# Kernel tuning notes

Hardware: AMD Instinct MI355X
Metric: run time of the kernel (lower is better)

Reference implementation:

```python
import jax, jax.numpy as jnp
import numpy as np

IN_NC, OUT_NC, K = 64, 64, 3          # adc_in_nc, adc_out_nc, adc_kers
FC_SIZE = 512
FMN0, FMN1 = 512, 512
GROUP_FC = 4
CNN_PARA = IN_NC * OUT_NC * K * K + OUT_NC  # 36928
B, H, W = 16, 128, 128


def setup_inputs() -> dict:
    key = jax.random.key(0)
    ks = jax.random.split(key, 8)
    s = 0.05
    return {
        "x": jax.random.normal(ks[0], (B, IN_NC, H, W), jnp.float32),
        "fc_in": jax.random.normal(ks[1], (B, FC_SIZE), jnp.float32),
        "w1": jax.random.normal(ks[2], (FMN0, FC_SIZE), jnp.float32) * s,
        "b1": jax.random.normal(ks[3], (FMN0,), jnp.float32) * s,
        "w2": jax.random.normal(ks[4], (FMN1, FMN0), jnp.float32) * s,
        "b2": jax.random.normal(ks[5], (FMN1,), jnp.float32) * s,
        # grouped 1x1 conv1d: [groups, out_per_group, in_per_group]
        "w3": jax.random.normal(ks[6], (GROUP_FC, CNN_PARA // GROUP_FC, FMN1 // GROUP_FC), jnp.float32) * s,
        "b3": jax.random.normal(ks[7], (CNN_PARA,), jnp.float32) * s,
        "splits": B,
    }


def _fmn(fc_in, w1, b1, w2, b2, w3, b3):
    # per-sample MLP (Conv1d with kernel 1 over length-1 sequence)
    h = jax.nn.relu(fc_in @ w1.T + b1)                      # [B, FMN0]
    h = jax.nn.relu(h @ w2.T + b2)                          # [B, FMN1]
    hg = h.reshape(h.shape[0], GROUP_FC, -1)                # [B, G, FMN1/G]
    o = jnp.einsum('bgi,goi->bgo', hg, w3)                  # [B, G, CNN_PARA/G]
    o = o.reshape(h.shape[0], -1) + b3                      # [B, CNN_PARA]
    return jax.nn.relu(o)


def reference(x, fc_in, w1, b1, w2, b2, w3, b3, splits):
    batch, C, Hx, Wx = x.shape
    wb = _fmn(fc_in, w1, b1, w2, b2, w3, b3)                # [B, CNN_PARA]
    weight = wb[:, :-OUT_NC].reshape(splits * OUT_NC, IN_NC, K, K)
    bias = wb[:, -OUT_NC:].reshape(-1)                      # [B*OUT_NC]
    # per-sample conv via grouped conv (groups = batch), VALID padding, stride 1
    y = jax.lax.conv_general_dilated(
        x.reshape(1, batch * C, Hx, Wx), weight,
        window_strides=(1, 1), padding='VALID',
        feature_group_count=batch,
        dimension_numbers=('NCHW', 'OIHW', 'NCHW'))          # [1, B*OUT, H', W']
    y = y + bias[None, :, None, None]
    # match torch conv3d output shape [1, B*OUT, 1, H', W']
    return y.reshape(1, batch * OUT_NC, 1, y.shape[-2], y.shape[-1])
```

## Files before the change

### kernel.cpp

```cpp
#include <hip/hip_runtime.h>
#include <hip/hip_bf16.h>

constexpr int BATCH   = 16;
constexpr int IN_NC   = 64;
constexpr int OUT_NC  = 64;
constexpr int KS      = 3;
constexpr int FC      = 512;
constexpr int GROUPS  = 4;
constexpr int CNN_PARA = IN_NC * OUT_NC * KS * KS + OUT_NC;
constexpr int PER_G   = CNN_PARA / GROUPS;
constexpr int IN_PER_G = FC / GROUPS;
constexpr int H = 128, W = 128;
constexpr int HO = 126, WO = 126;
constexpr int PIX = HO * WO;
constexpr int WCOUNT = IN_NC * OUT_NC * KS * KS;
constexpr int HW = H * W;

typedef __attribute__((ext_vector_type(8))) short short8;
typedef __attribute__((ext_vector_type(4))) float f32x4;

static __device__ __forceinline__ short bf16_bits(float f) {
    __hip_bfloat16 h = __float2bfloat16(f);
    union { __hip_bfloat16 h; short s; } u; u.h = h;
    return u.s;
}

__global__ __launch_bounds__(256) void mlp_layer(
    const float* __restrict__ in, const float* __restrict__ w,
    const float* __restrict__ bias, float* __restrict__ out)
{
    int gtid = blockIdx.x * blockDim.x + threadIdx.x;
    int wave = gtid >> 6;
    int lane = threadIdx.x & 63;
    if (wave >= BATCH * FC) return;
    int b = wave >> 9;
    int o = wave & (FC - 1);
    const float* in_row = in + b * FC;
    const float* w_row  = w + (size_t)o * FC;
    float acc = 0.f;
#pragma unroll
    for (int i = 0; i < FC / 64; ++i) acc += in_row[lane + i * 64] * w_row[lane + i * 64];
#pragma unroll
    for (int off = 32; off > 0; off >>= 1) acc += __shfl_down(acc, off, 64);
    if (lane == 0) {
        float v = acc + bias[o];
        out[b * FC + o] = v > 0.f ? v : 0.f;
    }
}

__global__ __launch_bounds__(256) void grouped_fc(
    const float* __restrict__ h2, const float* __restrict__ w3,
    const float* __restrict__ b3, float* __restrict__ wb)
{
    __shared__ float hs[BATCH * FC];
    int tid = threadIdx.x;
    for (int i = tid; i < BATCH * FC; i += blockDim.x) hs[i] = h2[i];
    __syncthreads();

    int j = blockIdx.x * blockDim.x + tid;
    if (j >= CNN_PARA) return;
    int g  = j / PER_G;
    int jj = j - g * PER_G;
    const float4* wrow = (const float4*)(w3 + ((size_t)g * PER_G + jj) * IN_PER_G);
    float acc[BATCH];
#pragma unroll
    for (int b = 0; b < BATCH; ++b) acc[b] = 0.f;
    const float* hbase = hs + g * IN_PER_G;
#pragma unroll 4
    for (int i4 = 0; i4 < IN_PER_G / 4; ++i4) {
        float4 wv = wrow[i4];
#pragma unroll
        for (int b = 0; b < BATCH; ++b) {
            const float* hb = hbase + b * FC + i4 * 4;
            acc[b] += wv.x * hb[0] + wv.y * hb[1] + wv.z * hb[2] + wv.w * hb[3];
        }
    }
    float bv = b3[j];
#pragma unroll
    for (int b = 0; b < BATCH; ++b) {
        float v = acc[b] + bv;
        wb[(size_t)b * CNN_PARA + j] = v > 0.f ? v : 0.f;
    }
}

__global__ __launch_bounds__(256) void conv_w_transpose(
    const float* __restrict__ wb, __hip_bfloat16* __restrict__ wT)
{
    int idx = blockIdx.x * blockDim.x + threadIdx.x;
    if (idx >= BATCH * 9 * 64 * 64) return;
    int b    = idx / (9 * 4096);
    int r    = idx % (9 * 4096);
    int kykx = r >> 12;
    int q    = r & 4095;
    int oc   = q >> 6;
    int ic   = q & 63;
    float v = wb[(size_t)b * CNN_PARA + (oc * 64 + ic) * 9 + kykx];
    union { __hip_bfloat16 h; short s; } u; u.s = bf16_bits(v);
    wT[idx] = u.h;
}

__global__ __launch_bounds__(256) void conv_x_transpose(
    const float* __restrict__ x, __hip_bfloat16* __restrict__ xT)
{
    __shared__ float lds[64][129];
    int blk = blockIdx.x;
    int b = blk >> 7, h = blk & 127;
    int tid = threadIdx.x;

    const float* xrow = x + (size_t)b * IN_NC * HW + (size_t)h * W;
#pragma unroll 8
    for (int it = 0; it < 32; ++it) {
        int ic = it * 2 + (tid >> 7);
        int w  = tid & 127;
        lds[ic][w] = xrow[(size_t)ic * HW + w];
    }
    __syncthreads();

    __hip_bfloat16* dst = xT + ((size_t)(b * 128 + h)) * (128 * 64);
#pragma unroll
    for (int i = 0; i < 4; ++i) {
        int chunk = i * 256 + tid;
        int w = chunk >> 3, oct = chunk & 7;
        short8 v;
#pragma unroll
        for (int j = 0; j < 8; ++j) v[j] = bf16_bits(lds[oct * 8 + j][w]);
        *(short8*)(dst + (size_t)w * 64 + oct * 8) = v;
    }
}

__global__ __launch_bounds__(256) void conv_mfma(
    const __hip_bfloat16* __restrict__ xT,
    const __hip_bfloat16* __restrict__ wT,
    const float* __restrict__ wb,
    float* __restrict__ out)
{
    int blk = blockIdx.x;
    int b   = blk / 63;
    int oyp = blk % 63;
    int tid = threadIdx.x;
    int wv = tid >> 6, l = tid & 63;
    int mrow  = wv & 1;
    int nhalf = wv >> 1;
    int row = oyp * 2 + nhalf;
    int l15 = l & 15, l4 = l >> 4;

    f32x4 acc[2][8];
#pragma unroll
    for (int mf = 0; mf < 2; ++mf)
#pragma unroll
        for (int nf = 0; nf < 8; ++nf) acc[mf][nf] = (f32x4)0.f;

#pragma unroll
    for (int kykx = 0; kykx < 9; ++kykx) {
        int ky = kykx / 3, kx = kykx % 3;
        const __hip_bfloat16* wtile = wT + (size_t)(b * 9 + kykx) * 4096;
        const __hip_bfloat16* xbase =
            xT + ((size_t)(b * 128 + row + ky) * 128 + kx) * 64;
#pragma unroll
        for (int ks = 0; ks < 2; ++ks) {
            int ic0 = ks * 32 + l4 * 8;
            short8 a0 = *(const short8*)(wtile + (mrow * 32 + l15) * 64 + ic0);
            short8 a1 = *(const short8*)(wtile + (mrow * 32 + 16 + l15) * 64 + ic0);
#pragma unroll
            for (int nf = 0; nf < 8; ++nf) {
                int ox = nf * 16 + l15;
                short8 bf = *(const short8*)(xbase + (size_t)ox * 64 + ic0);
                acc[0][nf] = __builtin_amdgcn_mfma_f32_16x16x32_bf16(a0, bf, acc[0][nf], 0, 0, 0);
                acc[1][nf] = __builtin_amdgcn_mfma_f32_16x16x32_bf16(a1, bf, acc[1][nf], 0, 0, 0);
            }
        }
    }

    float bias[2][4];
#pragma unroll
    for (int mf = 0; mf < 2; ++mf)
#pragma unroll
        for (int r = 0; r < 4; ++r)
            bias[mf][r] = wb[(size_t)b * CNN_PARA + WCOUNT + mrow * 32 + mf * 16 + l4 * 4 + r];

#pragma unroll
    for (int mf = 0; mf < 2; ++mf)
#pragma unroll
        for (int nf = 0; nf < 8; ++nf) {
            int ox = nf * 16 + l15;
            if (ox >= WO) continue;
#pragma unroll
            for (int r = 0; r < 4; ++r) {
                int oc = mrow * 32 + mf * 16 + l4 * 4 + r;
                out[((size_t)(b * 64 + oc)) * PIX + row * WO + ox] = acc[mf][nf][r] + bias[mf][r];
            }
        }
}

__global__ __launch_bounds__(256) void conv_direct(
    const float* __restrict__ x, const float* __restrict__ wb,
    float* __restrict__ out)
{
    constexpr int NBLK = (PIX + 255) / 256;
    __shared__ float wsm[IN_NC * 9];
    __shared__ float bias_s;
    int bid  = blockIdx.x;
    int tile = bid % NBLK;
    int boc  = bid / NBLK;
    int b = boc >> 6, oc = boc & 63;
    int tid = threadIdx.x;
    const float* wsrc = wb + (size_t)b * CNN_PARA + oc * (IN_NC * 9);
    if (tid < IN_NC * 9 / 4) ((float4*)wsm)[tid] = ((const float4*)wsrc)[tid];
    if (tid == 0) bias_s = wb[(size_t)b * CNN_PARA + WCOUNT + oc];
    __syncthreads();
    int p = tile * 256 + tid;
    if (p >= PIX) return;
    int oy = p / WO, ox = p - oy * WO;
    const float* xb = x + (size_t)b * IN_NC * HW + oy * W + ox;
    float acc = bias_s;
    for (int ic = 0; ic < IN_NC; ++ic) {
        const float* xr = xb + ic * HW;
        const float* wr = wsm + ic * 9;
#pragma unroll
        for (int ky = 0; ky < 3; ++ky) {
            acc += xr[ky * W + 0] * wr[ky * 3 + 0];
            acc += xr[ky * W + 1] * wr[ky * 3 + 1];
            acc += xr[ky * W + 2] * wr[ky * 3 + 2];
        }
    }
    out[(size_t)boc * PIX + p] = acc;
}

extern "C" void kernel_launch(void* const* d_in, const int* in_sizes, int n_in,
                              void* d_out, int out_size, void* d_ws, size_t ws_size,
                              hipStream_t stream) {
    const float* x     = (const float*)d_in[0];
    const float* fc_in = (const float*)d_in[1];
    const float* w1    = (const float*)d_in[2];
    const float* b1    = (const float*)d_in[3];
    const float* w2    = (const float*)d_in[4];
    const float* b2    = (const float*)d_in[5];
    const float* w3    = (const float*)d_in[6];
    const float* b3    = (const float*)d_in[7];
    float* out = (float*)d_out;

    const size_t off_h1 = 0;
    const size_t off_h2 = off_h1 + (size_t)BATCH * FC * 4;
    const size_t off_wb = off_h2 + (size_t)BATCH * FC * 4;
    const size_t off_wT = off_wb + (size_t)BATCH * CNN_PARA * 4;
    const size_t off_xT = off_wT + (size_t)BATCH * 9 * 4096 * 2;
    const size_t xT_bytes = (size_t)BATCH * 128 * 128 * 64 * 2 + 16384;
    const size_t need = off_xT + xT_bytes;

    float* h1 = (float*)((char*)d_ws + off_h1);
    float* h2 = (float*)((char*)d_ws + off_h2);
    float* wb = (float*)((char*)d_ws + off_wb);

    mlp_layer<<<2048, 256, 0, stream>>>(fc_in, w1, b1, h1);
    mlp_layer<<<2048, 256, 0, stream>>>(h1, w2, b2, h2);
    grouped_fc<<<(CNN_PARA + 255) / 256, 256, 0, stream>>>(h2, w3, b3, wb);

    if (ws_size >= need) {
        __hip_bfloat16* wT = (__hip_bfloat16*)((char*)d_ws + off_wT);
        __hip_bfloat16* xT = (__hip_bfloat16*)((char*)d_ws + off_xT);
        conv_w_transpose<<<(BATCH * 9 * 4096 + 255) / 256, 256, 0, stream>>>(wb, wT);
        conv_x_transpose<<<BATCH * 128, 256, 0, stream>>>(x, xT);
        conv_mfma<<<BATCH * 63, 256, 0, stream>>>(xT, wT, wb, out);
    } else {
        conv_direct<<<BATCH * OUT_NC * ((PIX + 255) / 256), 256, 0, stream>>>(x, wb, out);
    }
}
```

Baseline: 270.6 us.

## Restructure MLP kernels for batch reuse and retile conv MFMA with XCD swizzle

The MLP layers now stage all batch activations in shared memory and have each wave compute one output neuron for all 16 samples, so each weight row is read once instead of once per sample. The grouped FC switches to a wave-per-output layout with coalesced weight loads and shuffle reductions. The conv MFMA kernel changes from a 2x8 to a 4x4 fragment tile per wave to improve operand reuse, adds an occupancy hint, and remaps block indices across XCDs. This brings more shuffle reductions, launches one block per four outputs in grouped_fc, and adds register pressure in the conv kernel.

```diff
diff --git a/kernel.cpp b/kernel.cpp
--- a/kernel.cpp
+++ b/kernel.cpp
@@ -20,66 +20,83 @@
 typedef __attribute__((ext_vector_type(4))) float f32x4;
 
 static __device__ __forceinline__ short bf16_bits(float f) {
-    __hip_bfloat16 h = __float2bfloat16(f);
-    union { __hip_bfloat16 h; short s; } u; u.h = h;
+    union { __hip_bfloat16 h; short s; } u;
+    u.h = __float2bfloat16(f);
     return u.s;
 }
 
 __global__ __launch_bounds__(256) void mlp_layer(
-    const float* __restrict__ in, const float* __restrict__ w,
-    const float* __restrict__ bias, float* __restrict__ out)
-{
-    int gtid = blockIdx.x * blockDim.x + threadIdx.x;
-    int wave = gtid >> 6;
-    int lane = threadIdx.x & 63;
-    if (wave >= BATCH * FC) return;
-    int b = wave >> 9;
-    int o = wave & (FC - 1);
-    const float* in_row = in + b * FC;
-    const float* w_row  = w + (size_t)o * FC;
-    float acc = 0.f;
-#pragma unroll
-    for (int i = 0; i < FC / 64; ++i) acc += in_row[lane + i * 64] * w_row[lane + i * 64];
-#pragma unroll
-    for (int off = 32; off > 0; off >>= 1) acc += __shfl_down(acc, off, 64);
-    if (lane == 0) {
-        float v = acc + bias[o];
-        out[b * FC + o] = v > 0.f ? v : 0.f;
+    const float* __restrict__ in,
+    const float* __restrict__ w,
+    const float* __restrict__ bias,
+    float* __restrict__ out)
+{
+    __shared__ float hs[BATCH * FC];
+    int tid = threadIdx.x;
+    for (int i = tid; i < BATCH * FC; i += 256) hs[i] = in[i];
+    __syncthreads();
+
+    int o = blockIdx.x * 4 + (tid >> 6);
+    int l = tid & 63;
+    const float4* wrow = (const float4*)(w + (size_t)o * FC + l * 8);
+    float4 w0 = wrow[0], w1 = wrow[1];
+
+    float acc[BATCH];
+#pragma unroll
+    for (int b = 0; b < BATCH; ++b) {
+        const float4* hp = (const float4*)(hs + b * FC + l * 8);
+        float4 h0 = hp[0], h1 = hp[1];
+        acc[b] = w0.x * h0.x + w0.y * h0.y + w0.z * h0.z + w0.w * h0.w
+               + w1.x * h1.x + w1.y * h1.y + w1.z * h1.z + w1.w * h1.w;
+    }
+#pragma unroll
+    for (int off = 32; off > 0; off >>= 1)
+#pragma unroll
+        for (int b = 0; b < BATCH; ++b)
+            acc[b] += __shfl_down(acc[b], off, 64);
+    if (l == 0) {
+        float bv = bias[o];
+#pragma unroll
+        for (int b = 0; b < BATCH; ++b) {
+            float v = acc[b] + bv;
+            out[b * FC + o] = v > 0.f ? v : 0.f;
+        }
     }
 }
 
 __global__ __launch_bounds__(256) void grouped_fc(
-    const float* __restrict__ h2, const float* __restrict__ w3,
-    const float* __restrict__ b3, float* __restrict__ wb)
+    const float* __restrict__ h2,
+    const float* __restrict__ w3,
+    const float* __restrict__ b3,
+    float* __restrict__ wb)
 {
     __shared__ float hs[BATCH * FC];
     int tid = threadIdx.x;
-    for (int i = tid; i < BATCH * FC; i += blockDim.x) hs[i] = h2[i];
-    __syncthreads();
-
-    int j = blockIdx.x * blockDim.x + tid;
-    if (j >= CNN_PARA) return;
-    int g  = j / PER_G;
-    int jj = j - g * PER_G;
-    const float4* wrow = (const float4*)(w3 + ((size_t)g * PER_G + jj) * IN_PER_G);
+    for (int i = tid; i < BATCH * FC; i += 256) hs[i] = h2[i];
+    __syncthreads();
+
+    int j = blockIdx.x * 4 + (tid >> 6);
+    int l = tid & 63;
+    int g = j / PER_G;
+    const float2 wv = *(const float2*)(w3 + (size_t)j * IN_PER_G + l * 2);
+    const float* hbase = hs + g * IN_PER_G + l * 2;
+
     float acc[BATCH];
 #pragma unroll
-    for (int b = 0; b < BATCH; ++b) acc[b] = 0.f;
-    const float* hbase = hs + g * IN_PER_G;
-#pragma unroll 4
-    for (int i4 = 0; i4 < IN_PER_G / 4; ++i4) {
-        float4 wv = wrow[i4];
+    for (int b = 0; b < BATCH; ++b)
+        acc[b] = wv.x * hbase[b * FC] + wv.y * hbase[b * FC + 1];
+#pragma unroll
+    for (int off = 32; off > 0; off >>= 1)
+#pragma unroll
+        for (int b = 0; b < BATCH; ++b)
+            acc[b] += __shfl_down(acc[b], off, 64);
+    if (l == 0) {
+        float bv = b3[j];
 #pragma unroll
         for (int b = 0; b < BATCH; ++b) {
-            const float* hb = hbase + b * FC + i4 * 4;
-            acc[b] += wv.x * hb[0] + wv.y * hb[1] + wv.z * hb[2] + wv.w * hb[3];
-        }
-    }
-    float bv = b3[j];
-#pragma unroll
-    for (int b = 0; b < BATCH; ++b) {
-        float v = acc[b] + bv;
-        wb[(size_t)b * CNN_PARA + j] = v > 0.f ? v : 0.f;
+            float v = acc[b] + bv;
+            wb[(size_t)b * CNN_PARA + j] = v > 0.f ? v : 0.f;
+        }
     }
 }
 
@@ -87,7 +104,7 @@
     const float* __restrict__ wb, __hip_bfloat16* __restrict__ wT)
 {
     int idx = blockIdx.x * blockDim.x + threadIdx.x;
-    if (idx >= BATCH * 9 * 64 * 64) return;
+    if (idx >= BATCH * 9 * 4096) return;
     int b    = idx / (9 * 4096);
     int r    = idx % (9 * 4096);
     int kykx = r >> 12;
@@ -128,66 +145,72 @@
     }
 }
 
-__global__ __launch_bounds__(256) void conv_mfma(
+__global__ __launch_bounds__(256, 4) void conv_mfma(
     const __hip_bfloat16* __restrict__ xT,
     const __hip_bfloat16* __restrict__ wT,
     const float* __restrict__ wb,
     float* __restrict__ out)
 {
-    int blk = blockIdx.x;
-    int b   = blk / 63;
-    int oyp = blk % 63;
+    int wg   = blockIdx.x;
+    int sblk = (wg & 7) * 126 + (wg >> 3);
+    int b    = sblk / 63;
+    int rp   = sblk % 63;
+
     int tid = threadIdx.x;
     int wv = tid >> 6, l = tid & 63;
-    int mrow  = wv & 1;
-    int nhalf = wv >> 1;
-    int row = oyp * 2 + nhalf;
     int l15 = l & 15, l4 = l >> 4;
-
-    f32x4 acc[2][8];
-#pragma unroll
-    for (int mf = 0; mf < 2; ++mf)
-#pragma unroll
-        for (int nf = 0; nf < 8; ++nf) acc[mf][nf] = (f32x4)0.f;
+    int row = rp * 2 + (wv >> 1);
+    int px0 = (wv & 1) * 64;
+
+    f32x4 acc[4][4];
+#pragma unroll
+    for (int mf = 0; mf < 4; ++mf)
+#pragma unroll
+        for (int nf = 0; nf < 4; ++nf) acc[mf][nf] = (f32x4)0.f;
 
 #pragma unroll
     for (int kykx = 0; kykx < 9; ++kykx) {
         int ky = kykx / 3, kx = kykx % 3;
         const __hip_bfloat16* wtile = wT + (size_t)(b * 9 + kykx) * 4096;
-        const __hip_bfloat16* xbase =
+        const __hip_bfloat16* xrow =
             xT + ((size_t)(b * 128 + row + ky) * 128 + kx) * 64;
 #pragma unroll
         for (int ks = 0; ks < 2; ++ks) {
             int ic0 = ks * 32 + l4 * 8;
-            short8 a0 = *(const short8*)(wtile + (mrow * 32 + l15) * 64 + ic0);
-            short8 a1 = *(const short8*)(wtile + (mrow * 32 + 16 + l15) * 64 + ic0);
-#pragma unroll
-            for (int nf = 0; nf < 8; ++nf) {
-                int ox = nf * 16 + l15;
-                short8 bf = *(const short8*)(xbase + (size_t)ox * 64 + ic0);
-                acc[0][nf] = __builtin_amdgcn_mfma_f32_16x16x32_bf16(a0, bf, acc[0][nf], 0, 0, 0);
-                acc[1][nf] = __builtin_amdgcn_mfma_f32_16x16x32_bf16(a1, bf, acc[1][nf], 0, 0, 0);
+            short8 A[4];
+#pragma unroll
+            for (int mf = 0; mf < 4; ++mf)
+                A[mf] = *(const short8*)(wtile + (mf * 16 + l15) * 64 + ic0);
+#pragma unroll
+            for (int nf = 0; nf < 4; ++nf) {
+                int ox = px0 + nf * 16 + l15;
+                short8 bf = *(const short8*)(xrow + (size_t)ox * 64 + ic0);
+#pragma unroll
+                for (int mf = 0; mf < 4; ++mf)
+                    acc[mf][nf] = __builtin_amdgcn_mfma_f32_16x16x32_bf16(
+                        A[mf], bf, acc[mf][nf], 0, 0, 0);
             }
         }
     }
 
-    float bias[2][4];
-#pragma unroll
-    for (int mf = 0; mf < 2; ++mf)
+    float bias[4][4];
+#pragma unroll
+    for (int mf = 0; mf < 4; ++mf)
 #pragma unroll
         for (int r = 0; r < 4; ++r)
-            bias[mf][r] = wb[(size_t)b * CNN_PARA + WCOUNT + mrow * 32 + mf * 16 + l4 * 4 + r];
-
-#pragma unroll
-    for (int mf = 0; mf < 2; ++mf)
-#pragma unroll
-        for (int nf = 0; nf < 8; ++nf) {
-            int ox = nf * 16 + l15;
+            bias[mf][r] = wb[(size_t)b * CNN_PARA + WCOUNT + mf * 16 + l4 * 4 + r];
+
+#pragma unroll
+    for (int mf = 0; mf < 4; ++mf)
+#pragma unroll
+        for (int nf = 0; nf < 4; ++nf) {
+            int ox = px0 + nf * 16 + l15;
             if (ox >= WO) continue;
 #pragma unroll
             for (int r = 0; r < 4; ++r) {
-                int oc = mrow * 32 + mf * 16 + l4 * 4 + r;
-                out[((size_t)(b * 64 + oc)) * PIX + row * WO + ox] = acc[mf][nf][r] + bias[mf][r];
+                int oc = mf * 16 + l4 * 4 + r;
+                out[((size_t)(b * 64 + oc)) * PIX + row * WO + ox]
+                    = acc[mf][nf][r] + bias[mf][r];
             }
         }
 }
@@ -251,9 +274,9 @@
     float* h2 = (float*)((char*)d_ws + off_h2);
     float* wb = (float*)((char*)d_ws + off_wb);
 
-    mlp_layer<<<2048, 256, 0, stream>>>(fc_in, w1, b1, h1);
-    mlp_layer<<<2048, 256, 0, stream>>>(h1, w2, b2, h2);
-    grouped_fc<<<(CNN_PARA + 255) / 256, 256, 0, stream>>>(h2, w3, b3, wb);
+    mlp_layer<<<FC / 4, 256, 0, stream>>>(fc_in, w1, b1, h1);
+    mlp_layer<<<FC / 4, 256, 0, stream>>>(h1, w2, b2, h2);
+    grouped_fc<<<CNN_PARA / 4, 256, 0, stream>>>(h2, w3, b3, wb);
 
     if (ws_size >= need) {
         __hip_bfloat16* wT = (__hip_bfloat16*)((char*)d_ws + off_wT);
```

New measurement: 280.0 us. 1.03x slower.
